# Performance work log

Hardware: AMD Instinct MI355X
Metric: run time of the kernel (lower is better)

The kernel has to match this reference:

```python
import jax, jax.numpy as jnp
import numpy as np

D_IN = 1024
D_OUT = 1024
NUM_HEADS = 16
HEAD_DIM = D_OUT // NUM_HEADS
WINDOW = 256


def setup_inputs() -> dict:
    key = jax.random.key(0)
    ks = jax.random.split(key, 6)
    s = 0.02
    x = jax.random.normal(ks[0], (2, 2048, D_IN), dtype=jnp.float32)
    Wq = jax.random.normal(ks[1], (D_IN, D_OUT), dtype=jnp.float32) * s
    Wk = jax.random.normal(ks[2], (D_IN, D_OUT), dtype=jnp.float32) * s
    Wv = jax.random.normal(ks[3], (D_IN, D_OUT), dtype=jnp.float32) * s
    Wo = jax.random.normal(ks[4], (D_OUT, D_OUT), dtype=jnp.float32) * s
    bo = jnp.zeros((D_OUT,), dtype=jnp.float32)
    return {"x": x, "Wq": Wq, "Wk": Wk, "Wv": Wv, "Wo": Wo, "bo": bo}


def reference(x, Wq, Wk, Wv, Wo, bo):
    b, s, _ = x.shape
    # project and split heads: [b, h, s, hd]
    def heads(t):
        return t.reshape(b, s, NUM_HEADS, HEAD_DIM).transpose(0, 2, 1, 3)
    q = heads(x @ Wq)
    k = heads(x @ Wk)
    v = heads(x @ Wv)
    scores = jnp.einsum('bhqd,bhkd->bhqk', q, k) / jnp.sqrt(jnp.float32(HEAD_DIM))
    # symmetric sliding-window band: |i - j| <= WINDOW
    i = jnp.arange(s)
    band = jnp.abs(i[:, None] - i[None, :]) <= WINDOW  # [s, s]
    scores = jnp.where(band[None, None], scores, -jnp.inf)
    probs = jax.nn.softmax(scores, axis=-1)  # dropout=0.0 -> identity
    ctx = jnp.einsum('bhqk,bhkd->bhqd', probs, v)
    ctx = ctx.transpose(0, 2, 1, 3).reshape(b, s, D_OUT)
    return ctx @ Wo + bo
```

## Files before the change

kernel.cpp:

```cpp
#include <hip/hip_runtime.h>
#include <hip/hip_bf16.h>

typedef __bf16 bf16_t;
typedef __bf16 bf16x8 __attribute__((ext_vector_type(8)));
typedef __bf16 bf16x4 __attribute__((ext_vector_type(4)));
typedef float  f32x4  __attribute__((ext_vector_type(4)));

#define SEQ    2048
#define BATCH  2
#define NHEAD  16
#define HDIM   64
#define DMODEL 1024
#define WIN    256
#define QSCALE 0.1803368801111244f

__device__ __forceinline__ void async_load16(const void* g, void* l) {
    __builtin_amdgcn_global_load_lds(
        (const __attribute__((address_space(1))) char*)(uintptr_t)g,
        (__attribute__((address_space(3))) char*)(uintptr_t)l, 16, 0, 0);
}

__global__ void cast_x_kernel(const float* __restrict__ x, bf16_t* __restrict__ xb, int n4) {
    int i = blockIdx.x * blockDim.x + threadIdx.x;
    if (i >= n4) return;
    float4 v = ((const float4*)x)[i];
    bf16x4 o;
    o[0] = (bf16_t)v.x; o[1] = (bf16_t)v.y; o[2] = (bf16_t)v.z; o[3] = (bf16_t)v.w;
    ((bf16x4*)xb)[i] = o;
}

__global__ void transpose_w_kernel(const float* __restrict__ Wq, const float* __restrict__ Wk,
                                   const float* __restrict__ Wv, const float* __restrict__ Wo,
                                   bf16_t* __restrict__ Wt) {
    __shared__ float tile[32][33];
    const float* W = (blockIdx.z == 0) ? Wq : (blockIdx.z == 1) ? Wk : (blockIdx.z == 2) ? Wv : Wo;
    bf16_t* out = Wt + (size_t)blockIdx.z * DMODEL * DMODEL;
    int k0 = blockIdx.y * 32, n0 = blockIdx.x * 32;
    int tx = threadIdx.x, ty = threadIdx.y;
#pragma unroll
    for (int i = 0; i < 4; i++)
        tile[ty + i * 8][tx] = W[(size_t)(k0 + ty + i * 8) * DMODEL + n0 + tx];
    __syncthreads();
#pragma unroll
    for (int i = 0; i < 4; i++)
        out[(size_t)(n0 + ty + i * 8) * DMODEL + k0 + tx] = (bf16_t)tile[tx][ty + i * 8];
}

__global__ __launch_bounds__(256) void vtrans_kernel(const bf16_t* __restrict__ Vb,
                                                     bf16_t* __restrict__ Vt) {
    __shared__ bf16_t tile[64][65];
    const int bh = blockIdx.y, s0 = blockIdx.x * 64;
    const int tx = threadIdx.x, ty = threadIdx.y;
    const bf16_t* src = Vb + ((size_t)bh * SEQ + s0) * HDIM;
    bf16_t* dst = Vt + (size_t)bh * HDIM * SEQ + s0;
#pragma unroll
    for (int i = 0; i < 16; i++) {
        int row = i * 4 + ty;
        tile[row][tx] = src[(size_t)row * HDIM + tx];
    }
    __syncthreads();
#pragma unroll
    for (int i = 0; i < 16; i++) {
        int d = i * 4 + ty;
        dst[(size_t)d * SEQ + tx] = tile[tx][d];
    }
}

template <int EPI>
__global__ __launch_bounds__(256) void gemm_bt_kernel(
    const bf16_t* __restrict__ A, const bf16_t* __restrict__ Bt,
    bf16_t* __restrict__ Qb, bf16_t* __restrict__ Kb, bf16_t* __restrict__ Vb,
    float* __restrict__ Out, const float* __restrict__ bo, int K, int nPer) {
    __shared__ __attribute__((aligned(16))) bf16_t As[128 * 64];
    __shared__ __attribute__((aligned(16))) bf16_t Bs[128 * 64];
    const int tid = threadIdx.x;
    const int wave = tid >> 6, lane = tid & 63, quad = lane >> 4, l15 = lane & 15;
    const int wm = wave >> 1, wn = wave & 1;
    const int id = blockIdx.x, xcd = id & 7, t = id >> 3;
    const int m0 = (t / nPer) * 128, n0 = (xcd * nPer + t % nPer) * 128;

    f32x4 acc[4][4] = {};

    for (int kt = 0; kt < K; kt += 64) {
#pragma unroll
        for (int i = 0; i < 4; i++) {
            int v = tid + i * 256;
            int row = v >> 3, c = (v & 7) ^ (row & 7);
            async_load16(A + (size_t)(m0 + row) * K + kt + c * 8, (char*)As + (size_t)v * 16);
            async_load16(Bt + (size_t)(n0 + row) * K + kt + c * 8, (char*)Bs + (size_t)v * 16);
        }
        __syncthreads();
#pragma unroll
        for (int kk = 0; kk < 64; kk += 32) {
            bf16x8 am[4], bn[4];
#pragma unroll
            for (int i = 0; i < 4; i++) {
                int row = wm * 64 + i * 16 + l15;
                int ch = ((kk >> 3) + quad) ^ (row & 7);
                am[i] = *(const bf16x8*)&As[row * 64 + ch * 8];
            }
#pragma unroll
            for (int j = 0; j < 4; j++) {
                int row = wn * 64 + j * 16 + l15;
                int ch = ((kk >> 3) + quad) ^ (row & 7);
                bn[j] = *(const bf16x8*)&Bs[row * 64 + ch * 8];
            }
#pragma unroll
            for (int i = 0; i < 4; i++)
#pragma unroll
                for (int j = 0; j < 4; j++)
                    acc[i][j] = __builtin_amdgcn_mfma_f32_16x16x32_bf16(am[i], bn[j], acc[i][j], 0, 0, 0);
        }
        __syncthreads();
    }

#pragma unroll
    for (int i = 0; i < 4; i++)
#pragma unroll
        for (int j = 0; j < 4; j++)
#pragma unroll
            for (int r = 0; r < 4; r++) {
                int mg = m0 + wm * 64 + i * 16 + quad * 4 + r;
                int ng = n0 + wn * 64 + j * 16 + l15;
                float v = acc[i][j][r];
                if (EPI == 0) {
                    int sel = ng >> 10, nl = ng & 1023, h = nl >> 6, d = nl & 63;
                    int b = mg >> 11, s = mg & 2047;
                    size_t idx = ((size_t)((b * NHEAD + h) * SEQ) + s) * HDIM + d;
                    if (sel == 0)      Qb[idx] = (bf16_t)(v * QSCALE);
                    else if (sel == 1) Kb[idx] = (bf16_t)v;
                    else               Vb[idx] = (bf16_t)v;
                } else {
                    Out[(size_t)mg * DMODEL + ng] = v + bo[ng];
                }
            }
}

__global__ __launch_bounds__(512) void attn_kernel(
    const bf16_t* __restrict__ Qb, const bf16_t* __restrict__ Kb,
    const bf16_t* __restrict__ Vt, bf16_t* __restrict__ ctx) {
    __shared__ __attribute__((aligned(16))) bf16_t Ks[2][64 * 64];
    __shared__ __attribute__((aligned(16))) bf16_t Vs[2][64 * 64];
    __shared__ __attribute__((aligned(16))) bf16_t Plds[8][16][72];
    const int tid = threadIdx.x;
    const int wave = tid >> 6, lane = tid & 63, quad = lane >> 4, l15 = lane & 15;

    const int id = blockIdx.x;
    const int b = id >> 8, h = (id >> 4) & 15, Q0 = (id & 15) << 7;
    const int qbase = Q0 + wave * 16;
    const int wqt = (Q0 >> 6) + (wave >> 2);

    const bf16_t* Qp = Qb + (size_t)(b * NHEAD + h) * SEQ * HDIM;
    const bf16_t* Kp = Kb + (size_t)(b * NHEAD + h) * SEQ * HDIM;
    const bf16_t* Vp = Vt + (size_t)(b * NHEAD + h) * HDIM * SEQ;

    bf16x8 qa0 = *(const bf16x8*)(Qp + (size_t)(qbase + l15) * HDIM + quad * 8);
    bf16x8 qa1 = *(const bf16x8*)(Qp + (size_t)(qbase + l15) * HDIM + 32 + quad * 8);

    bf16x8 ones;
#pragma unroll
    for (int j = 0; j < 8; j++) ones[j] = (bf16_t)1.0f;

    f32x4 O[4] = {};
    f32x4 lacc = {};

    const int base_t = Q0 >> 6;
    const int bt0 = (base_t - 4 > 0) ? base_t - 4 : 0;
    const int bt1 = (base_t + 5 < SEQ / 64 - 1) ? base_t + 5 : SEQ / 64 - 1;

    auto stage = [&](int kt, int buf) {
        const int k0 = kt * 64;
        int v = tid;
        int row = v >> 3, c = (v & 7) ^ (row & 7);
        async_load16(Kp + (size_t)(k0 + row) * HDIM + c * 8, (char*)&Ks[buf][0] + (size_t)v * 16);
        async_load16(Vp + (size_t)row * SEQ + k0 + c * 8, (char*)&Vs[buf][0] + (size_t)v * 16);
    };

    stage(bt0, 0);
    int cb = 0;
    for (int kt = bt0; kt <= bt1; kt++) {
        __syncthreads();
        if (kt < bt1) stage(kt + 1, cb ^ 1);
        const int dt = kt - wqt;
        if (dt >= -4 && dt <= 4) {
            const int k0 = kt * 64;
            f32x4 s[4];
#pragma unroll
            for (int c = 0; c < 4; c++) {
                int row = c * 16 + l15;
                bf16x8 kb0 = *(const bf16x8*)&Ks[cb][row * 64 + (quad ^ (row & 7)) * 8];
                bf16x8 kb1 = *(const bf16x8*)&Ks[cb][row * 64 + ((quad + 4) ^ (row & 7)) * 8];
                f32x4 a = {};
                a = __builtin_amdgcn_mfma_f32_16x16x32_bf16(qa0, kb0, a, 0, 0, 0);
                a = __builtin_amdgcn_mfma_f32_16x16x32_bf16(qa1, kb1, a, 0, 0, 0);
                s[c] = a;
            }
            const bool edge = (dt == -4 || dt == 4);
#pragma unroll
            for (int c = 0; c < 4; c++)
#pragma unroll
                for (int r = 0; r < 4; r++) {
                    float sv = s[c][r];
                    if (edge) {
                        int i = qbase + quad * 4 + r;
                        int j = k0 + c * 16 + l15;
                        int dd = i - j; dd = (dd < 0) ? -dd : dd;
                        if (dd > WIN) sv = -1e30f;
                    }
                    Plds[wave][quad * 4 + r][c * 16 + l15] = (bf16_t)__builtin_exp2f(sv);
                }
            bf16x8 pa0 = *(const bf16x8*)&Plds[wave][l15][quad * 8];
            bf16x8 pa1 = *(const bf16x8*)&Plds[wave][l15][32 + quad * 8];
            lacc = __builtin_amdgcn_mfma_f32_16x16x32_bf16(pa0, ones, lacc, 0, 0, 0);
            lacc = __builtin_amdgcn_mfma_f32_16x16x32_bf16(pa1, ones, lacc, 0, 0, 0);
#pragma unroll
            for (int d = 0; d < 4; d++) {
                int row = d * 16 + l15;
                bf16x8 vb0 = *(const bf16x8*)&Vs[cb][row * 64 + (quad ^ (row & 7)) * 8];
                bf16x8 vb1 = *(const bf16x8*)&Vs[cb][row * 64 + ((quad + 4) ^ (row & 7)) * 8];
                O[d] = __builtin_amdgcn_mfma_f32_16x16x32_bf16(pa0, vb0, O[d], 0, 0, 0);
                O[d] = __builtin_amdgcn_mfma_f32_16x16x32_bf16(pa1, vb1, O[d], 0, 0, 0);
            }
        }
        __syncthreads();
        cb ^= 1;
    }

#pragma unroll
    for (int r = 0; r < 4; r++) {
        float inv = 1.0f / lacc[r];
        int i = qbase + quad * 4 + r;
#pragma unroll
        for (int d = 0; d < 4; d++) {
            float v = O[d][r] * inv;
            ctx[((size_t)(b * SEQ + i)) * DMODEL + h * HDIM + d * 16 + l15] = (bf16_t)v;
        }
    }
}

extern "C" void kernel_launch(void* const* d_in, const int* in_sizes, int n_in,
                              void* d_out, int out_size, void* d_ws, size_t ws_size,
                              hipStream_t stream) {
    const float* x  = (const float*)d_in[0];
    const float* Wq = (const float*)d_in[1];
    const float* Wk = (const float*)d_in[2];
    const float* Wv = (const float*)d_in[3];
    const float* Wo = (const float*)d_in[4];
    const float* bo = (const float*)d_in[5];
    float* out = (float*)d_out;

    const size_t MTOK = (size_t)BATCH * SEQ;
    bf16_t* xb  = (bf16_t*)d_ws;
    bf16_t* Wt  = xb + MTOK * DMODEL;
    bf16_t* Qb  = Wt + (size_t)4 * DMODEL * DMODEL;
    bf16_t* Kb  = Qb + MTOK * DMODEL;
    bf16_t* Vt  = Kb + MTOK * DMODEL;
    bf16_t* ctx = Vt + MTOK * DMODEL;
    bf16_t* Vb  = ctx;

    cast_x_kernel<<<dim3((MTOK * DMODEL / 4 + 255) / 256), dim3(256), 0, stream>>>(
        x, xb, (int)(MTOK * DMODEL / 4));
    transpose_w_kernel<<<dim3(32, 32, 4), dim3(32, 8), 0, stream>>>(Wq, Wk, Wv, Wo, Wt);
    gemm_bt_kernel<0><<<dim3(768), dim3(256), 0, stream>>>(
        xb, Wt, Qb, Kb, Vb, nullptr, nullptr, DMODEL, 3);
    vtrans_kernel<<<dim3(32, 32), dim3(64, 4), 0, stream>>>(Vb, Vt);
    attn_kernel<<<dim3(512), dim3(512), 0, stream>>>(Qb, Kb, Vt, ctx);
    gemm_bt_kernel<1><<<dim3(256), dim3(256), 0, stream>>>(
        ctx, Wt + (size_t)3 * DMODEL * DMODEL, nullptr, nullptr, nullptr, out, bo, DMODEL, 1);
}
```

Baseline: 174.4 us.

## Fuse prep kernels, write V transposed from QKV GEMM epilogue, retile output GEMM

Merges the x cast and the weight transpose into a single prep launch. The V transpose kernel is removed: the QKV GEMM now stages V tiles through LDS and writes them already transposed with 16-byte stores. The output projection GEMM uses 64-row tiles so it launches 512 blocks instead of 256, giving better CU occupancy. Together these drop two launches and one round trip of V through global memory, at the cost of a heavier epilogue with an extra barrier for V blocks.

```diff
diff --git a/kernel.cpp b/kernel.cpp
--- a/kernel.cpp
+++ b/kernel.cpp
@@ -20,79 +20,69 @@
         (__attribute__((address_space(3))) char*)(uintptr_t)l, 16, 0, 0);
 }
 
-__global__ void cast_x_kernel(const float* __restrict__ x, bf16_t* __restrict__ xb, int n4) {
-    int i = blockIdx.x * blockDim.x + threadIdx.x;
-    if (i >= n4) return;
-    float4 v = ((const float4*)x)[i];
-    bf16x4 o;
-    o[0] = (bf16_t)v.x; o[1] = (bf16_t)v.y; o[2] = (bf16_t)v.z; o[3] = (bf16_t)v.w;
-    ((bf16x4*)xb)[i] = o;
-}
-
-__global__ void transpose_w_kernel(const float* __restrict__ Wq, const float* __restrict__ Wk,
-                                   const float* __restrict__ Wv, const float* __restrict__ Wo,
-                                   bf16_t* __restrict__ Wt) {
+__global__ void prep_kernel(const float* __restrict__ x,
+                            const float* __restrict__ Wq, const float* __restrict__ Wk,
+                            const float* __restrict__ Wv, const float* __restrict__ Wo,
+                            bf16_t* __restrict__ xb, bf16_t* __restrict__ Wt) {
     __shared__ float tile[32][33];
-    const float* W = (blockIdx.z == 0) ? Wq : (blockIdx.z == 1) ? Wk : (blockIdx.z == 2) ? Wv : Wo;
-    bf16_t* out = Wt + (size_t)blockIdx.z * DMODEL * DMODEL;
-    int k0 = blockIdx.y * 32, n0 = blockIdx.x * 32;
-    int tx = threadIdx.x, ty = threadIdx.y;
-#pragma unroll
-    for (int i = 0; i < 4; i++)
-        tile[ty + i * 8][tx] = W[(size_t)(k0 + ty + i * 8) * DMODEL + n0 + tx];
-    __syncthreads();
-#pragma unroll
-    for (int i = 0; i < 4; i++)
-        out[(size_t)(n0 + ty + i * 8) * DMODEL + k0 + tx] = (bf16_t)tile[tx][ty + i * 8];
-}
-
-__global__ __launch_bounds__(256) void vtrans_kernel(const bf16_t* __restrict__ Vb,
-                                                     bf16_t* __restrict__ Vt) {
-    __shared__ bf16_t tile[64][65];
-    const int bh = blockIdx.y, s0 = blockIdx.x * 64;
+    const int z = blockIdx.z;
     const int tx = threadIdx.x, ty = threadIdx.y;
-    const bf16_t* src = Vb + ((size_t)bh * SEQ + s0) * HDIM;
-    bf16_t* dst = Vt + (size_t)bh * HDIM * SEQ + s0;
-#pragma unroll
-    for (int i = 0; i < 16; i++) {
-        int row = i * 4 + ty;
-        tile[row][tx] = src[(size_t)row * HDIM + tx];
-    }
-    __syncthreads();
-#pragma unroll
-    for (int i = 0; i < 16; i++) {
-        int d = i * 4 + ty;
-        dst[(size_t)d * SEQ + tx] = tile[tx][d];
-    }
-}
-
-template <int EPI>
+    if (z < 4) {
+        const float* W = (z == 0) ? Wq : (z == 1) ? Wk : (z == 2) ? Wv : Wo;
+        bf16_t* out = Wt + (size_t)z * DMODEL * DMODEL;
+        int k0 = blockIdx.y * 32, n0 = blockIdx.x * 32;
+#pragma unroll
+        for (int i = 0; i < 4; i++)
+            tile[ty + i * 8][tx] = W[(size_t)(k0 + ty + i * 8) * DMODEL + n0 + tx];
+        __syncthreads();
+#pragma unroll
+        for (int i = 0; i < 4; i++)
+            out[(size_t)(n0 + ty + i * 8) * DMODEL + k0 + tx] = (bf16_t)tile[tx][ty + i * 8];
+    } else {
+        int blk = (z - 4) * 1024 + blockIdx.y * 32 + blockIdx.x;
+        int i = blk * 256 + ty * 32 + tx;
+        float4 v = ((const float4*)x)[i];
+        bf16x4 o;
+        o[0] = (bf16_t)v.x; o[1] = (bf16_t)v.y; o[2] = (bf16_t)v.z; o[3] = (bf16_t)v.w;
+        ((bf16x4*)xb)[i] = o;
+    }
+}
+
+template <int EPI, int BM>
 __global__ __launch_bounds__(256) void gemm_bt_kernel(
     const bf16_t* __restrict__ A, const bf16_t* __restrict__ Bt,
-    bf16_t* __restrict__ Qb, bf16_t* __restrict__ Kb, bf16_t* __restrict__ Vb,
+    bf16_t* __restrict__ Qb, bf16_t* __restrict__ Kb, bf16_t* __restrict__ Vt,
     float* __restrict__ Out, const float* __restrict__ bo, int K, int nPer) {
-    __shared__ __attribute__((aligned(16))) bf16_t As[128 * 64];
-    __shared__ __attribute__((aligned(16))) bf16_t Bs[128 * 64];
+    constexpr int JN = (BM == 128) ? 4 : 2;
+    __shared__ __attribute__((aligned(16))) bf16_t smem[BM * 64 + 128 * 64];
+    bf16_t* As = smem;
+    bf16_t* Bs = smem + BM * 64;
     const int tid = threadIdx.x;
     const int wave = tid >> 6, lane = tid & 63, quad = lane >> 4, l15 = lane & 15;
-    const int wm = wave >> 1, wn = wave & 1;
+    const int wm = (BM == 128) ? (wave >> 1) : 0;
+    const int wn = (BM == 128) ? (wave & 1) : wave;
     const int id = blockIdx.x, xcd = id & 7, t = id >> 3;
-    const int m0 = (t / nPer) * 128, n0 = (xcd * nPer + t % nPer) * 128;
-
-    f32x4 acc[4][4] = {};
+    const int m0 = (t / nPer) * BM, n0 = (xcd * nPer + t % nPer) * 128;
+
+    f32x4 acc[4][JN] = {};
 
     for (int kt = 0; kt < K; kt += 64) {
+#pragma unroll
+        for (int i = 0; i < BM / 32; i++) {
+            int v = tid + i * 256;
+            int row = v >> 3, c = (v & 7) ^ (row & 7);
+            async_load16(A + (size_t)(m0 + row) * K + kt + c * 8, (char*)As + (size_t)v * 16);
+        }
 #pragma unroll
         for (int i = 0; i < 4; i++) {
             int v = tid + i * 256;
             int row = v >> 3, c = (v & 7) ^ (row & 7);
-            async_load16(A + (size_t)(m0 + row) * K + kt + c * 8, (char*)As + (size_t)v * 16);
             async_load16(Bt + (size_t)(n0 + row) * K + kt + c * 8, (char*)Bs + (size_t)v * 16);
         }
         __syncthreads();
 #pragma unroll
         for (int kk = 0; kk < 64; kk += 32) {
-            bf16x8 am[4], bn[4];
+            bf16x8 am[4], bn[JN];
 #pragma unroll
             for (int i = 0; i < 4; i++) {
                 int row = wm * 64 + i * 16 + l15;
@@ -100,40 +90,80 @@
                 am[i] = *(const bf16x8*)&As[row * 64 + ch * 8];
             }
 #pragma unroll
-            for (int j = 0; j < 4; j++) {
-                int row = wn * 64 + j * 16 + l15;
+            for (int j = 0; j < JN; j++) {
+                int row = wn * JN * 16 + j * 16 + l15;
                 int ch = ((kk >> 3) + quad) ^ (row & 7);
                 bn[j] = *(const bf16x8*)&Bs[row * 64 + ch * 8];
             }
 #pragma unroll
             for (int i = 0; i < 4; i++)
 #pragma unroll
-                for (int j = 0; j < 4; j++)
+                for (int j = 0; j < JN; j++)
                     acc[i][j] = __builtin_amdgcn_mfma_f32_16x16x32_bf16(am[i], bn[j], acc[i][j], 0, 0, 0);
         }
         __syncthreads();
     }
 
-#pragma unroll
-    for (int i = 0; i < 4; i++)
-#pragma unroll
-        for (int j = 0; j < 4; j++)
-#pragma unroll
-            for (int r = 0; r < 4; r++) {
-                int mg = m0 + wm * 64 + i * 16 + quad * 4 + r;
-                int ng = n0 + wn * 64 + j * 16 + l15;
-                float v = acc[i][j][r];
-                if (EPI == 0) {
-                    int sel = ng >> 10, nl = ng & 1023, h = nl >> 6, d = nl & 63;
+    if (EPI == 1) {
+#pragma unroll
+        for (int i = 0; i < 4; i++)
+#pragma unroll
+            for (int j = 0; j < JN; j++)
+#pragma unroll
+                for (int r = 0; r < 4; r++) {
+                    int mg = m0 + wm * 64 + i * 16 + quad * 4 + r;
+                    int ng = n0 + wn * JN * 16 + j * 16 + l15;
+                    Out[(size_t)mg * DMODEL + ng] = acc[i][j][r] + bo[ng];
+                }
+        return;
+    }
+
+    const int sel = n0 >> 10;
+    if (sel < 2) {
+#pragma unroll
+        for (int i = 0; i < 4; i++)
+#pragma unroll
+            for (int j = 0; j < JN; j++)
+#pragma unroll
+                for (int r = 0; r < 4; r++) {
+                    int mg = m0 + wm * 64 + i * 16 + quad * 4 + r;
+                    int ng = n0 + wn * JN * 16 + j * 16 + l15;
+                    int h = (ng & 1023) >> 6, d = ng & 63;
                     int b = mg >> 11, s = mg & 2047;
                     size_t idx = ((size_t)((b * NHEAD + h) * SEQ) + s) * HDIM + d;
-                    if (sel == 0)      Qb[idx] = (bf16_t)(v * QSCALE);
-                    else if (sel == 1) Kb[idx] = (bf16_t)v;
-                    else               Vb[idx] = (bf16_t)v;
-                } else {
-                    Out[(size_t)mg * DMODEL + ng] = v + bo[ng];
+                    float v = acc[i][j][r];
+                    if (sel == 0) Qb[idx] = (bf16_t)(v * QSCALE);
+                    else          Kb[idx] = (bf16_t)v;
                 }
-            }
+    } else {
+        bf16_t* T = smem;
+#pragma unroll
+        for (int i = 0; i < 4; i++)
+#pragma unroll
+            for (int j = 0; j < JN; j++) {
+                int nl = wn * JN * 16 + j * 16 + l15;
+                int mlc = wm * 16 + i * 4 + quad;
+                bf16x4 p;
+#pragma unroll
+                for (int r = 0; r < 4; r++) p[r] = (bf16_t)acc[i][j][r];
+                *(bf16x4*)&T[nl * 128 + ((mlc ^ (nl & 31)) << 2)] = p;
+            }
+        __syncthreads();
+        const int h0 = (n0 & 1023) >> 6;
+        const int b = m0 >> 11, sbase = m0 & 2047;
+#pragma unroll
+        for (int it = 0; it < 8; it++) {
+            int idx = tid + it * 256;
+            int nl = idx >> 4, sc = idx & 15;
+            bf16x4 lo = *(const bf16x4*)&T[nl * 128 + (((2 * sc) ^ (nl & 31)) << 2)];
+            bf16x4 hi = *(const bf16x4*)&T[nl * 128 + (((2 * sc + 1) ^ (nl & 31)) << 2)];
+            bf16x8 w;
+#pragma unroll
+            for (int e = 0; e < 4; e++) { w[e] = lo[e]; w[e + 4] = hi[e]; }
+            int h = h0 + (nl >> 6), d = nl & 63;
+            *(bf16x8*)(Vt + ((size_t)(b * NHEAD + h) * HDIM + d) * SEQ + sbase + sc * 8) = w;
+        }
+    }
 }
 
 __global__ __launch_bounds__(512) void attn_kernel(
@@ -256,15 +286,11 @@
     bf16_t* Kb  = Qb + MTOK * DMODEL;
     bf16_t* Vt  = Kb + MTOK * DMODEL;
     bf16_t* ctx = Vt + MTOK * DMODEL;
-    bf16_t* Vb  = ctx;
-
-    cast_x_kernel<<<dim3((MTOK * DMODEL / 4 + 255) / 256), dim3(256), 0, stream>>>(
-        x, xb, (int)(MTOK * DMODEL / 4));
-    transpose_w_kernel<<<dim3(32, 32, 4), dim3(32, 8), 0, stream>>>(Wq, Wk, Wv, Wo, Wt);
-    gemm_bt_kernel<0><<<dim3(768), dim3(256), 0, stream>>>(
-        xb, Wt, Qb, Kb, Vb, nullptr, nullptr, DMODEL, 3);
-    vtrans_kernel<<<dim3(32, 32), dim3(64, 4), 0, stream>>>(Vb, Vt);
+
+    prep_kernel<<<dim3(32, 32, 8), dim3(32, 8), 0, stream>>>(x, Wq, Wk, Wv, Wo, xb, Wt);
+    gemm_bt_kernel<0, 128><<<dim3(768), dim3(256), 0, stream>>>(
+        xb, Wt, Qb, Kb, Vt, nullptr, nullptr, DMODEL, 3);
     attn_kernel<<<dim3(512), dim3(512), 0, stream>>>(Qb, Kb, Vt, ctx);
-    gemm_bt_kernel<1><<<dim3(256), dim3(256), 0, stream>>>(
+    gemm_bt_kernel<1, 64><<<dim3(512), dim3(256), 0, stream>>>(
         ctx, Wt + (size_t)3 * DMODEL * DMODEL, nullptr, nullptr, nullptr, out, bo, DMODEL, 1);
 }
```

Result: no change. 174.0 us (-0.2%).
